# Kernel tuning notes

Hardware: AMD Instinct MI355X
Metric: run time of the kernel (lower is better)

Reference implementation:

```python
import jax, jax.numpy as jnp
import numpy as np

B, N = 32, 512
NFEAT, NHID, NCLASS, NHEADS = 128, 64, 128, 8
WORK_D, SUB_D = 32, 32
H1, H2, OUT_D = 256, 256, 512
ALPHA = 0.2
NEG = -9e15


def setup_inputs() -> dict:
    key = jax.random.key(0)
    ks = jax.random.split(key, 16)
    return {
        "graph_inf": jax.random.normal(ks[0], (B, N, NFEAT), jnp.float32),
        "graph_matrix": jax.random.randint(ks[1], (B, N, N), 0, 2, jnp.int32),
        "masks": jnp.ones((B, N), jnp.float32),
        "node_order": jax.random.randint(ks[2], (B,), 0, N, jnp.int64),
        "work": jax.random.normal(ks[3], (B, WORK_D), jnp.float32),
        "subtask": jax.random.normal(ks[4], (B, SUB_D), jnp.float32),
        # GAT head params
        "W_heads": jax.random.normal(ks[5], (NHEADS, NFEAT, NHID), jnp.float32) * 0.1,
        "a_heads": jax.random.normal(ks[6], (NHEADS, 2 * NHID), jnp.float32) * 0.1,
        "W_out": jax.random.normal(ks[7], (NHID * NHEADS, NCLASS), jnp.float32) * 0.05,
        "a_out": jax.random.normal(ks[8], (2 * NCLASS,), jnp.float32) * 0.1,
        # MLP encoder params
        "fc1_w": jax.random.normal(ks[9], (NCLASS + WORK_D + SUB_D, H1), jnp.float32) * 0.07,
        "fc1_b": jnp.zeros((H1,), jnp.float32),
        "fc2_w": jax.random.normal(ks[10], (H1, H2), jnp.float32) * 0.06,
        "fc2_b": jnp.zeros((H2,), jnp.float32),
        "fc3_w": jax.random.normal(ks[11], (H2, OUT_D), jnp.float32) * 0.06,
        "fc3_b": jnp.zeros((OUT_D,), jnp.float32),
    }


def _gat_layer(Wh, a1, a2, adj, masks):
    # Wh: [B,N,F]; additive GAT score e_ij = leakyrelu(a1.Wh_i + a2.Wh_j)
    s1 = Wh @ a1  # [B,N]
    s2 = Wh @ a2  # [B,N]
    e = jax.nn.leaky_relu(s1[:, :, None] + s2[:, None, :], ALPHA)  # [B,N,N]
    att = jax.nn.softmax(jnp.where(adj > 0, e, NEG), axis=2)
    h_prime = jnp.einsum('bnm,bmf->bnf', att, Wh)
    return h_prime * masks[:, :, None]


def reference(graph_inf, graph_matrix, masks, node_order, work, subtask,
              W_heads, a_heads, W_out, a_out,
              fc1_w, fc1_b, fc2_w, fc2_b, fc3_w, fc3_b):
    adj = graph_matrix
    # multi-head GAT layer (concat=True -> ELU)
    def head(Wk, ak):
        Wh = jnp.einsum('bnf,fo->bno', graph_inf, Wk)
        return jax.nn.elu(_gat_layer(Wh, ak[:NHID], ak[NHID:], adj, masks))
    xh = jax.vmap(head)(W_heads, a_heads)  # [H,B,N,NHID]
    x = jnp.transpose(xh, (1, 2, 0, 3)).reshape(B, N, NHEADS * NHID)
    # output GAT layer (concat=False)
    Wh = jnp.einsum('bnf,fo->bno', x, W_out)
    x = _gat_layer(Wh, a_out[:NCLASS], a_out[NCLASS:], adj, masks)
    x = x * masks[:, :, None]
    # select subtask node per batch element
    selected = x[jnp.arange(B), node_order]  # [B,NCLASS]
    inf = jnp.concatenate([selected, work, subtask], axis=1)
    h = jax.nn.relu(inf @ fc1_w + fc1_b)
    h = jax.nn.relu(h @ fc2_w + fc2_b)
    out = h @ fc3_w + fc3_b
    return jax.nn.softmax(out, axis=-1)
```

## Files before the change

kernel.cpp:

```cpp
#include <hip/hip_runtime.h>

typedef unsigned short u16;
typedef unsigned int u32;
typedef unsigned long long u64;

typedef __bf16 bf16x8 __attribute__((ext_vector_type(8)));
typedef float f32x4 __attribute__((ext_vector_type(4)));

#define LOG2E 1.44269504088896340736f

__device__ __forceinline__ float b2f(u16 u) {
    u32 x = ((u32)u) << 16;
    return __builtin_bit_cast(float, x);
}
__device__ __forceinline__ u16 f2b(float f) {
    u32 u = __builtin_bit_cast(u32, f);
    u32 r = (u + 0x7fffu + ((u >> 16) & 1u)) >> 16;
    return (u16)r;
}
__device__ __forceinline__ float ld(const void* p, int i, bool bf) {
    return bf ? b2f(((const u16*)p)[i]) : ((const float*)p)[i];
}
__device__ __forceinline__ bool detect_bf16(const void* masks) {
    return ((const u16*)masks)[0] != 0;
}
__device__ __forceinline__ f32x4 mfma16(bf16x8 a, bf16x8 b, f32x4 c) {
    return __builtin_amdgcn_mfma_f32_16x16x32_bf16(a, b, c, 0, 0, 0);
}

__device__ __attribute__((aligned(256))) u32  g_adjm[16384 * 16];
__device__ __attribute__((aligned(256))) u16  g_BT1[512 * 128];
__device__ __attribute__((aligned(256))) u16  g_BT2[128 * 512];
__device__ __attribute__((aligned(256))) u16  g_Xc[32 * 512 * 128];
__device__ __attribute__((aligned(256))) u16  g_xb[16384 * 512];
__device__ __attribute__((aligned(256))) u16  g_Wh2[16384 * 128];
__device__ __attribute__((aligned(256))) float g_s1b[16384];
__device__ __attribute__((aligned(256))) float g_s2b[16384];
__device__ __attribute__((aligned(256))) u16  g_fc1T[256 * 192];
__device__ __attribute__((aligned(256))) u16  g_fc2T[256 * 256];
__device__ __attribute__((aligned(256))) u16  g_fc3T[512 * 256];
__device__ __attribute__((aligned(256))) u16  g_Ahi[32 * 192];
__device__ __attribute__((aligned(256))) u16  g_Alo[32 * 192];
__device__ __attribute__((aligned(256))) u16  g_H1hi[32 * 256];
__device__ __attribute__((aligned(256))) u16  g_H1lo[32 * 256];
__device__ __attribute__((aligned(256))) u16  g_H2hi[32 * 256];
__device__ __attribute__((aligned(256))) u16  g_H2lo[32 * 256];
__device__ __attribute__((aligned(256))) float g_logits[32 * 512];

__global__ __launch_bounds__(256) void prep_kernel(
    const int* __restrict__ adj, const void* __restrict__ Whd,
    const void* __restrict__ Wo, const void* __restrict__ Xin,
    const void* __restrict__ fc1w, const void* __restrict__ fc2w,
    const void* __restrict__ fc3w, const void* __restrict__ masks)
{
    const bool bf = detect_bf16(masks);
    const int blk = blockIdx.x;
    const int tid = threadIdx.x;
    if (blk < 1024) {
        int id = blk * 256 + tid;
        int row = id >> 4, w = id & 15;
        const int4* p = (const int4*)(adj + row * 512 + w * 32);
        int4 v[8];
        #pragma unroll
        for (int s = 0; s < 8; ++s) v[s] = p[s];
        u32 word = 0;
        #pragma unroll
        for (int s = 0; s < 8; ++s) {
            u32 nib = (v[s].x > 0 ? 1u : 0u) | (v[s].y > 0 ? 2u : 0u) |
                      (v[s].z > 0 ? 4u : 0u) | (v[s].w > 0 ? 8u : 0u);
            word |= nib << (4 * s);
        }
        g_adjm[id] = word;
    } else if (blk < 1028) {
        int base = (blk - 1024) * 16384;
        for (int e = base + tid; e < base + 16384; e += 256) {
            int n = e >> 7, k = e & 127;
            g_BT1[e] = f2b(ld(Whd, (n >> 6) * 8192 + k * 64 + (n & 63), bf));
        }
    } else if (blk < 1032) {
        int base = (blk - 1028) * 16384;
        for (int e = base + tid; e < base + 16384; e += 256) {
            int n = e >> 9, k = e & 511;
            g_BT2[e] = f2b(ld(Wo, k * 128 + n, bf));
        }
    } else if (blk < 1288) {
        if (!bf) {
            int base = (blk - 1032) * 8192;
            for (int e = base + tid; e < base + 8192; e += 256)
                g_Xc[e] = f2b(((const float*)Xin)[e]);
        }
    } else if (blk < 1294) {
        int base = (blk - 1288) * 8192;
        for (int e = base + tid; e < base + 8192; e += 256) {
            int n = e / 192, k = e - n * 192;
            g_fc1T[e] = f2b(ld(fc1w, k * 256 + n, bf));
        }
    } else if (blk < 1302) {
        int base = (blk - 1294) * 8192;
        for (int e = base + tid; e < base + 8192; e += 256) {
            int n = e >> 8, k = e & 255;
            g_fc2T[e] = f2b(ld(fc2w, k * 256 + n, bf));
        }
    } else {
        int base = (blk - 1302) * 8192;
        for (int e = base + tid; e < base + 8192; e += 256) {
            int n = e >> 8, k = e & 255;
            g_fc3T[e] = f2b(ld(fc3w, k * 512 + n, bf));
        }
    }
}

__global__ __launch_bounds__(512, 1) void gat1_kernel(
    const void* __restrict__ Xin, const void* __restrict__ a_heads,
    const void* __restrict__ masks)
{
    __shared__ __attribute__((aligned(16))) u16 WhL[64 * 520];
    __shared__ __attribute__((aligned(16))) u16 As[64 * 136];
    __shared__ __attribute__((aligned(16))) u16 XcL[128 * 136];
    __shared__ float s1p[4][512];
    __shared__ float s2p[4][512];
    __shared__ float E2s[512];
    __shared__ float E2ps[512];

    const bool bf = detect_bf16(masks);
    const int tid = threadIdx.x;
    const int w = tid >> 6, lane = tid & 63;
    const int c = lane & 15, q = lane >> 4;
    const int h  = blockIdx.x & 7;
    const int b  = blockIdx.x >> 3;

    const u16* Bsrc = bf ? (const u16*)Xin : g_Xc;

    {
        int r = tid >> 3, seg = (tid & 7) * 16;
        const u16* src = g_BT1 + (h * 64 + r) * 128 + seg;
        *(uint4*)&As[r * 136 + seg] = *(const uint4*)src;
        *(uint4*)&As[r * 136 + seg + 8] = *(const uint4*)(src + 8);
    }

    const int wm = w & 3, wn = w >> 2;
    float a1v[4], a2v[4];
    #pragma unroll
    for (int i = 0; i < 4; ++i) {
        int o = wm * 16 + q * 4 + i;
        a1v[i] = ld(a_heads, h * 128 + o, bf);
        a2v[i] = ld(a_heads, h * 128 + 64 + o, bf);
    }

    for (int chunk = 0; chunk < 4; ++chunk) {
        __syncthreads();
        {
            int r = tid >> 2, seg = (tid & 3) * 32;
            const u16* src = Bsrc + (b * 512 + chunk * 128 + r) * 128 + seg;
            u16* dst = &XcL[r * 136 + seg];
            *(uint4*)dst = *(const uint4*)src;
            *(uint4*)(dst + 8) = *(const uint4*)(src + 8);
            *(uint4*)(dst + 16) = *(const uint4*)(src + 16);
            *(uint4*)(dst + 24) = *(const uint4*)(src + 24);
        }
        __syncthreads();
        f32x4 cacc[4] = {};
        #pragma unroll
        for (int kt = 0; kt < 4; ++kt) {
            bf16x8 af = *(const bf16x8*)&As[(wm * 16 + c) * 136 + kt * 32 + q * 8];
            #pragma unroll
            for (int nt = 0; nt < 4; ++nt) {
                bf16x8 bv = *(const bf16x8*)&XcL[(wn * 64 + nt * 16 + c) * 136 + kt * 32 + q * 8];
                cacc[nt] = mfma16(af, bv, cacc[nt]);
            }
        }
        #pragma unroll
        for (int nt = 0; nt < 4; ++nt) {
            const int ncol = chunk * 128 + wn * 64 + nt * 16 + c;
            float p1 = 0.f, p2 = 0.f;
            #pragma unroll
            for (int i = 0; i < 4; ++i) {
                float v = cacc[nt][i];
                WhL[(wm * 16 + q * 4 + i) * 520 + ncol] = f2b(v);
                p1 += v * a1v[i];
                p2 += v * a2v[i];
            }
            p1 += __shfl_xor(p1, 16); p1 += __shfl_xor(p1, 32);
            p2 += __shfl_xor(p2, 16); p2 += __shfl_xor(p2, 32);
            if (lane < 16) {
                int n = chunk * 128 + wn * 64 + nt * 16 + lane;
                s1p[wm][n] = p1;
                s2p[wm][n] = p2;
            }
        }
    }
    __syncthreads();
    {
        float s2v = (s2p[0][tid & 511] + s2p[1][tid & 511] +
                     s2p[2][tid & 511] + s2p[3][tid & 511]) * LOG2E;
        if (tid < 512) {
            E2s[tid]  = exp2f(s2v);
            E2ps[tid] = exp2f(0.2f * s2v);
        }
    }
    __syncthreads();

    const u32* adjb = g_adjm + b * 8192;
    const u32 bword = (c == 0) ? 0x3F803F80u : 0u;
    const uint4 bq = {bword, bword, bword, bword};
    const bf16x8 bone = __builtin_bit_cast(bf16x8, bq);

    float E1[4], E1p[4];
    #pragma unroll
    for (int g = 0; g < 4; ++g) {
        int r = w * 64 + g * 16 + c;
        float s1v = (s1p[0][r] + s1p[1][r] + s1p[2][r] + s1p[3][r]) * LOG2E;
        E1[g]  = exp2f(s1v);
        E1p[g] = exp2f(0.2f * s1v);
    }

    f32x4 acc[4][4] = {};
    f32x4 acc1[4] = {};
    const u16* lbase = &WhL[c * 520 + q * 8];

    for (int kc = 0; kc < 4; ++kc) {
        union { uint4 v; u32 a[4]; } wq[4];
        #pragma unroll
        for (int g = 0; g < 4; ++g)
            wq[g].v = *(const uint4*)(adjb + (w * 64 + g * 16 + c) * 16 + kc * 4);
        #pragma unroll
        for (int tl = 0; tl < 4; ++tl) {
            const int jb = kc * 128 + tl * 32 + q * 8;
            union { float4 v[2]; float f[8]; } e2r, e2pr;
            e2r.v[0]  = *(const float4*)&E2s[jb];
            e2r.v[1]  = *(const float4*)&E2s[jb + 4];
            e2pr.v[0] = *(const float4*)&E2ps[jb];
            e2pr.v[1] = *(const float4*)&E2ps[jb + 4];
            bf16x8 bfrag[4];
            #pragma unroll
            for (int nt = 0; nt < 4; ++nt)
                bfrag[nt] = *(const bf16x8*)(lbase + nt * 16 * 520 + kc * 128 + tl * 32);
            #pragma unroll
            for (int g = 0; g < 4; ++g) {
                u32 wbits = wq[g].a[tl] >> (q * 8);
                u32 pk[4];
                #pragma unroll
                for (int pi = 0; pi < 4; ++pi) {
                    float z0 = fmaxf(E1[g] * e2r.f[2 * pi],     E1p[g] * e2pr.f[2 * pi]);
                    float z1 = fmaxf(E1[g] * e2r.f[2 * pi + 1], E1p[g] * e2pr.f[2 * pi + 1]);
                    z0 = ((wbits >> (2 * pi)) & 1u) ? z0 : 0.f;
                    z1 = ((wbits >> (2 * pi + 1)) & 1u) ? z1 : 0.f;
                    pk[pi] = __builtin_amdgcn_perm(__builtin_bit_cast(u32, z1),
                                                   __builtin_bit_cast(u32, z0),
                                                   0x07060302u);
                }
                uint4 pkv = {pk[0], pk[1], pk[2], pk[3]};
                bf16x8 pv = __builtin_bit_cast(bf16x8, pkv);
                acc1[g] = mfma16(pv, bone, acc1[g]);
                #pragma unroll
                for (int nt = 0; nt < 4; ++nt)
                    acc[g][nt] = mfma16(pv, bfrag[nt], acc[g][nt]);
            }
        }
    }
    #pragma unroll
    for (int g = 0; g < 4; ++g) {
        const int R = w * 64 + g * 16;
        #pragma unroll
        for (int i = 0; i < 4; ++i) {
            float lr = __shfl(acc1[g][i], (lane & 48));
            float invr = (lr == 0.f) ? (1.f / 512.f) : (1.f / lr);
            const int row = R + q * 4 + i;
            float mk = ld(masks, b * 512 + row, bf);
            #pragma unroll
            for (int nt = 0; nt < 4; ++nt) {
                float v = acc[g][nt][i] * invr * mk;
                float o = v > 0.f ? v : (__expf(v) - 1.f);
                g_xb[(b * 512 + row) * 512 + h * 64 + nt * 16 + c] = f2b(o);
            }
        }
    }
}

__global__ __launch_bounds__(256, 2) void gemm2_kernel(
    const void* __restrict__ a_out, const void* __restrict__ masks)
{
    __shared__ __attribute__((aligned(16))) u16 Asl[64 * 72];
    __shared__ __attribute__((aligned(16))) u16 Bsl[128 * 72];
    const int tid = threadIdx.x;
    const int w = tid >> 6, lane = tid & 63;
    const int c = lane & 15, q = lane >> 4;
    const int tm = blockIdx.x * 64;
    const int rowA = tid >> 2, shA = (tid & 3) * 16;
    const int rowB = tid >> 1, shB = (tid & 1) * 32;
    f32x4 acc[8] = {};
    for (int kc = 0; kc < 512; kc += 64) {
        __syncthreads();
        const u16* Ag = g_xb + (tm + rowA) * 512 + kc + shA;
        *(uint4*)&Asl[rowA * 72 + shA] = *(const uint4*)Ag;
        *(uint4*)&Asl[rowA * 72 + shA + 8] = *(const uint4*)(Ag + 8);
        const u16* Bg = g_BT2 + rowB * 512 + kc + shB;
        #pragma unroll
        for (int s = 0; s < 4; ++s)
            *(uint4*)&Bsl[rowB * 72 + shB + 8 * s] = *(const uint4*)(Bg + 8 * s);
        __syncthreads();
        #pragma unroll
        for (int kt = 0; kt < 2; ++kt) {
            bf16x8 av = *(const bf16x8*)&Asl[(w * 16 + c) * 72 + kt * 32 + q * 8];
            #pragma unroll
            for (int ct = 0; ct < 8; ++ct) {
                bf16x8 bv = *(const bf16x8*)&Bsl[(ct * 16 + c) * 72 + kt * 32 + q * 8];
                acc[ct] = mfma16(av, bv, acc[ct]);
            }
        }
    }
    const bool bf = detect_bf16(masks);
    float a1v[8], a2v[8];
    #pragma unroll
    for (int ct = 0; ct < 8; ++ct) {
        a1v[ct] = ld(a_out, ct * 16 + c, bf);
        a2v[ct] = ld(a_out, 128 + ct * 16 + c, bf);
    }
    #pragma unroll
    for (int i = 0; i < 4; ++i) {
        float p1 = 0.f, p2 = 0.f;
        #pragma unroll
        for (int ct = 0; ct < 8; ++ct) {
            p1 += acc[ct][i] * a1v[ct];
            p2 += acc[ct][i] * a2v[ct];
        }
        #pragma unroll
        for (int off = 1; off < 16; off <<= 1) {
            p1 += __shfl_xor(p1, off);
            p2 += __shfl_xor(p2, off);
        }
        if (c == 0) {
            int m = tm + w * 16 + q * 4 + i;
            g_s1b[m] = p1 * LOG2E;
            g_s2b[m] = p2 * LOG2E;
        }
    }
    #pragma unroll
    for (int ct = 0; ct < 8; ++ct)
        #pragma unroll
        for (int i = 0; i < 4; ++i) {
            int m = tm + w * 16 + q * 4 + i;
            g_Wh2[m * 128 + ct * 16 + c] = f2b(acc[ct][i]);
        }
}

__global__ __launch_bounds__(256) void fin_att(
    const void* __restrict__ masks, const int* __restrict__ node_order,
    const void* __restrict__ workv, const void* __restrict__ subtaskv)
{
    __shared__ float att[512];
    __shared__ float parts[16][128];
    __shared__ float redl[4];

    const bool bf = detect_bf16(masks);
    const int b = blockIdx.x, t = threadIdx.x;
    const int lane = t & 63, wv = t >> 6;
    const int istar = node_order[b];

    const float s1v = g_s1b[b * 512 + istar];
    const u32* arow = g_adjm + (b * 512 + istar) * 16;
    float ssum = 0.f;
    #pragma unroll
    for (int rep = 0; rep < 2; ++rep) {
        int j = t + rep * 256;
        float e = s1v + g_s2b[b * 512 + j];
        e = fmaxf(e, 0.2f * e);
        float ex = ((arow[j >> 5] >> (j & 31)) & 1u) ? exp2f(e) : 0.f;
        att[j] = ex;
        ssum += ex;
    }
    for (int off = 1; off < 64; off <<= 1) ssum += __shfl_xor(ssum, off);
    if (lane == 0) redl[wv] = ssum;
    __syncthreads();
    float tot = redl[0] + redl[1] + redl[2] + redl[3];
    bool uni = (tot == 0.f);
    float inv = uni ? (1.f / 512.f) : (1.f / tot);

    const int og = t & 15, jg = t >> 4;
    float acc[8] = {};
    const u16* base = g_Wh2 + (b * 512 + jg * 32) * 128 + og * 8;
    #pragma unroll 8
    for (int j0 = 0; j0 < 32; ++j0) {
        float wgt = uni ? 1.f : att[jg * 32 + j0];
        union { u16 u[8]; uint4 v; } z;
        z.v = *(const uint4*)(base + j0 * 128);
        #pragma unroll
        for (int i = 0; i < 8; ++i) acc[i] += wgt * b2f(z.u[i]);
    }
    #pragma unroll
    for (int i = 0; i < 8; ++i) parts[jg][og * 8 + i] = acc[i];
    __syncthreads();
    float mk = ld(masks, b * 512 + istar, bf);
    if (t < 128) {
        float s = 0.f;
        #pragma unroll
        for (int jj = 0; jj < 16; ++jj) s += parts[jj][t];
        s *= inv * mk * mk;
        u16 hi = f2b(s);
        g_Ahi[b * 192 + t] = hi;
        g_Alo[b * 192 + t] = f2b(s - b2f(hi));
    } else if (t < 160) {
        g_Ahi[b * 192 + t] = bf ? ((const u16*)workv)[b * 32 + t - 128]
                                : f2b(((const float*)workv)[b * 32 + t - 128]);
        g_Alo[b * 192 + t] = 0;
    } else if (t < 192) {
        g_Ahi[b * 192 + t] = bf ? ((const u16*)subtaskv)[b * 32 + t - 160]
                                : f2b(((const float*)subtaskv)[b * 32 + t - 160]);
        g_Alo[b * 192 + t] = 0;
    }
}

template<int K, int NOUT, bool RELU>
__device__ __forceinline__ void mlp_body(
    const u16* __restrict__ Ahi, const u16* __restrict__ Alo,
    const u16* __restrict__ WT, const void* __restrict__ bias,
    u16* __restrict__ Ohi, u16* __restrict__ Olo, float* __restrict__ Of,
    const void* __restrict__ masks)
{
    const bool bf = detect_bf16(masks);
    const int t = threadIdx.x, w = t >> 6, lane = t & 63;
    const int c = lane & 15, q = lane >> 4;
    const int col = blockIdx.x * 64 + w * 16 + c;

    const u16* wp  = WT + col * K + q * 8;
    const u16* ahp = Ahi + c * K + q * 8;
    const u16* alp = Alo + c * K + q * 8;

    f32x4 acc0 = {}, acc1 = {};
    #pragma unroll
    for (int kt = 0; kt < K / 32; ++kt) {
        bf16x8 bw  = *(const bf16x8*)(wp + kt * 32);
        bf16x8 ah0 = *(const bf16x8*)(ahp + kt * 32);
        bf16x8 al0 = *(const bf16x8*)(alp + kt * 32);
        bf16x8 ah1 = *(const bf16x8*)(ahp + 16 * K + kt * 32);
        bf16x8 al1 = *(const bf16x8*)(alp + 16 * K + kt * 32);
        acc0 = mfma16(ah0, bw, acc0);
        acc0 = mfma16(al0, bw, acc0);
        acc1 = mfma16(ah1, bw, acc1);
        acc1 = mfma16(al1, bw, acc1);
    }
    float bs = ld(bias, col, bf);
    #pragma unroll
    for (int mt = 0; mt < 2; ++mt) {
        f32x4 a = mt ? acc1 : acc0;
        #pragma unroll
        for (int i = 0; i < 4; ++i) {
            int m = mt * 16 + q * 4 + i;
            float v = a[i] + bs;
            if (RELU) {
                v = fmaxf(v, 0.f);
                u16 hi = f2b(v);
                Ohi[m * NOUT + col] = hi;
                Olo[m * NOUT + col] = f2b(v - b2f(hi));
            } else {
                Of[m * NOUT + col] = v;
            }
        }
    }
}

__global__ __launch_bounds__(256) void mlp1_kernel(const void* bias, const void* masks) {
    mlp_body<192, 256, true>(g_Ahi, g_Alo, g_fc1T, bias, g_H1hi, g_H1lo, nullptr, masks);
}
__global__ __launch_bounds__(256) void mlp2_kernel(const void* bias, const void* masks) {
    mlp_body<256, 256, true>(g_H1hi, g_H1lo, g_fc2T, bias, g_H2hi, g_H2lo, nullptr, masks);
}
__global__ __launch_bounds__(256) void mlp3_kernel(const void* bias, const void* masks) {
    mlp_body<256, 512, false>(g_H2hi, g_H2lo, g_fc3T, bias, nullptr, nullptr, g_logits, masks);
}

__global__ __launch_bounds__(64) void softmax_kernel(
    const void* __restrict__ masks, void* __restrict__ out)
{
    const bool bf = detect_bf16(masks);
    const int row = blockIdx.x, lane = threadIdx.x;
    const float* lp = g_logits + row * 512 + lane * 8;
    float v[8];
    *(float4*)&v[0] = *(const float4*)lp;
    *(float4*)&v[4] = *(const float4*)(lp + 4);
    float mx = v[0];
    #pragma unroll
    for (int i = 1; i < 8; ++i) mx = fmaxf(mx, v[i]);
    for (int off = 1; off < 64; off <<= 1) mx = fmaxf(mx, __shfl_xor(mx, off));
    float e[8];
    float s = 0.f;
    #pragma unroll
    for (int i = 0; i < 8; ++i) { e[i] = __expf(v[i] - mx); s += e[i]; }
    for (int off = 1; off < 64; off <<= 1) s += __shfl_xor(s, off);
    float inv = 1.f / s;
    if (bf) {
        u16* o = (u16*)out + row * 512 + lane * 8;
        #pragma unroll
        for (int i = 0; i < 8; ++i) o[i] = f2b(e[i] * inv);
    } else {
        float* o = (float*)out + row * 512 + lane * 8;
        #pragma unroll
        for (int i = 0; i < 8; ++i) o[i] = e[i] * inv;
    }
}

extern "C" void kernel_launch(void* const* d_in, const int* in_sizes, int n_in,
                              void* d_out, int out_size, void* d_ws, size_t ws_size,
                              hipStream_t stream)
{
    const void* graph_inf    = d_in[0];
    const int*  graph_matrix = (const int*)d_in[1];
    const void* masks        = d_in[2];
    const int*  node_order   = (const int*)d_in[3];
    const void* work         = d_in[4];
    const void* subtask      = d_in[5];
    const void* W_heads      = d_in[6];
    const void* a_heads      = d_in[7];
    const void* W_out        = d_in[8];
    const void* a_out        = d_in[9];
    const void* fc1w         = d_in[10];
    const void* fc1b         = d_in[11];
    const void* fc2w         = d_in[12];
    const void* fc2b         = d_in[13];
    const void* fc3w         = d_in[14];
    const void* fc3b         = d_in[15];

    prep_kernel<<<dim3(1318), dim3(256), 0, stream>>>(graph_matrix, W_heads, W_out, graph_inf,
                                                      fc1w, fc2w, fc3w, masks);
    gat1_kernel<<<dim3(256), dim3(512), 0, stream>>>(graph_inf, a_heads, masks);
    gemm2_kernel<<<dim3(256), dim3(256), 0, stream>>>(a_out, masks);
    fin_att<<<dim3(32), dim3(256), 0, stream>>>(masks, node_order, work, subtask);
    mlp1_kernel<<<dim3(4), dim3(256), 0, stream>>>(fc1b, masks);
    mlp2_kernel<<<dim3(4), dim3(256), 0, stream>>>(fc2b, masks);
    mlp3_kernel<<<dim3(8), dim3(256), 0, stream>>>(fc3b, masks);
    softmax_kernel<<<dim3(32), dim3(64), 0, stream>>>(masks, d_out);
}
```

Baseline: 191.3 us.

## Double gat1 block to 1024 threads, prefetch X chunks in registers, remap block order

The GAT head kernel now runs 16 waves per block instead of 8, halving each wave's row groups in both the projection GEMM and the attention aggregation, which lowers register pressure and raises latency hiding. Loads of the next X chunk are issued into registers before the current chunk's MFMA work, so global latency overlaps compute. Block indexing puts batch in the low bits so consecutive blocks share a head's weights. The cost is more per-wave overhead from redundant B-fragment and E2 loads, and a higher chance of register spills under the 1024-thread bound.

```diff
diff --git a/kernel.cpp b/kernel.cpp
--- a/kernel.cpp
+++ b/kernel.cpp
@@ -110,7 +110,7 @@
     }
 }
 
-__global__ __launch_bounds__(512, 1) void gat1_kernel(
+__global__ __launch_bounds__(1024, 1) void gat1_kernel(
     const void* __restrict__ Xin, const void* __restrict__ a_heads,
     const void* __restrict__ masks)
 {
@@ -126,16 +126,14 @@
     const int tid = threadIdx.x;
     const int w = tid >> 6, lane = tid & 63;
     const int c = lane & 15, q = lane >> 4;
-    const int h  = blockIdx.x & 7;
-    const int b  = blockIdx.x >> 3;
+    const int b = blockIdx.x & 31;
+    const int h = blockIdx.x >> 5;
 
     const u16* Bsrc = bf ? (const u16*)Xin : g_Xc;
 
     {
-        int r = tid >> 3, seg = (tid & 7) * 16;
-        const u16* src = g_BT1 + (h * 64 + r) * 128 + seg;
-        *(uint4*)&As[r * 136 + seg] = *(const uint4*)src;
-        *(uint4*)&As[r * 136 + seg + 8] = *(const uint4*)(src + 8);
+        int r = tid >> 4, seg = (tid & 15) * 8;
+        *(uint4*)&As[r * 136 + seg] = *(const uint4*)(g_BT1 + (h * 64 + r) * 128 + seg);
     }
 
     const int wm = w & 3, wn = w >> 2;
@@ -147,31 +145,37 @@
         a2v[i] = ld(a_heads, h * 128 + 64 + o, bf);
     }
 
+    const int pr = tid >> 3, pseg = (tid & 7) * 16;
+    uint4 xr0, xr1;
+    {
+        const u16* src = Bsrc + (b * 512 + pr) * 128 + pseg;
+        xr0 = *(const uint4*)src;
+        xr1 = *(const uint4*)(src + 8);
+    }
+
     for (int chunk = 0; chunk < 4; ++chunk) {
         __syncthreads();
-        {
-            int r = tid >> 2, seg = (tid & 3) * 32;
-            const u16* src = Bsrc + (b * 512 + chunk * 128 + r) * 128 + seg;
-            u16* dst = &XcL[r * 136 + seg];
-            *(uint4*)dst = *(const uint4*)src;
-            *(uint4*)(dst + 8) = *(const uint4*)(src + 8);
-            *(uint4*)(dst + 16) = *(const uint4*)(src + 16);
-            *(uint4*)(dst + 24) = *(const uint4*)(src + 24);
+        *(uint4*)&XcL[pr * 136 + pseg] = xr0;
+        *(uint4*)&XcL[pr * 136 + pseg + 8] = xr1;
+        if (chunk < 3) {
+            const u16* src = Bsrc + (b * 512 + (chunk + 1) * 128 + pr) * 128 + pseg;
+            xr0 = *(const uint4*)src;
+            xr1 = *(const uint4*)(src + 8);
         }
         __syncthreads();
-        f32x4 cacc[4] = {};
+        f32x4 cacc[2] = {};
         #pragma unroll
         for (int kt = 0; kt < 4; ++kt) {
             bf16x8 af = *(const bf16x8*)&As[(wm * 16 + c) * 136 + kt * 32 + q * 8];
             #pragma unroll
-            for (int nt = 0; nt < 4; ++nt) {
-                bf16x8 bv = *(const bf16x8*)&XcL[(wn * 64 + nt * 16 + c) * 136 + kt * 32 + q * 8];
+            for (int nt = 0; nt < 2; ++nt) {
+                bf16x8 bv = *(const bf16x8*)&XcL[(wn * 32 + nt * 16 + c) * 136 + kt * 32 + q * 8];
                 cacc[nt] = mfma16(af, bv, cacc[nt]);
             }
         }
         #pragma unroll
-        for (int nt = 0; nt < 4; ++nt) {
-            const int ncol = chunk * 128 + wn * 64 + nt * 16 + c;
+        for (int nt = 0; nt < 2; ++nt) {
+            const int ncol = chunk * 128 + wn * 32 + nt * 16 + c;
             float p1 = 0.f, p2 = 0.f;
             #pragma unroll
             for (int i = 0; i < 4; ++i) {
@@ -183,7 +187,7 @@
             p1 += __shfl_xor(p1, 16); p1 += __shfl_xor(p1, 32);
             p2 += __shfl_xor(p2, 16); p2 += __shfl_xor(p2, 32);
             if (lane < 16) {
-                int n = chunk * 128 + wn * 64 + nt * 16 + lane;
+                int n = chunk * 128 + wn * 32 + nt * 16 + lane;
                 s1p[wm][n] = p1;
                 s2p[wm][n] = p2;
             }
@@ -191,12 +195,10 @@
     }
     __syncthreads();
     {
-        float s2v = (s2p[0][tid & 511] + s2p[1][tid & 511] +
-                     s2p[2][tid & 511] + s2p[3][tid & 511]) * LOG2E;
-        if (tid < 512) {
-            E2s[tid]  = exp2f(s2v);
-            E2ps[tid] = exp2f(0.2f * s2v);
-        }
+        int j = tid & 511;
+        float s2v = (s2p[0][j] + s2p[1][j] + s2p[2][j] + s2p[3][j]) * LOG2E;
+        if (tid < 512) E2s[j]  = exp2f(s2v);
+        else           E2ps[j] = exp2f(0.2f * s2v);
     }
     __syncthreads();
 
@@ -205,24 +207,24 @@
     const uint4 bq = {bword, bword, bword, bword};
     const bf16x8 bone = __builtin_bit_cast(bf16x8, bq);
 
-    float E1[4], E1p[4];
-    #pragma unroll
-    for (int g = 0; g < 4; ++g) {
-        int r = w * 64 + g * 16 + c;
+    float E1[2], E1p[2];
+    #pragma unroll
+    for (int g = 0; g < 2; ++g) {
+        int r = w * 32 + g * 16 + c;
         float s1v = (s1p[0][r] + s1p[1][r] + s1p[2][r] + s1p[3][r]) * LOG2E;
         E1[g]  = exp2f(s1v);
         E1p[g] = exp2f(0.2f * s1v);
     }
 
-    f32x4 acc[4][4] = {};
-    f32x4 acc1[4] = {};
+    f32x4 acc[2][4] = {};
+    f32x4 acc1[2] = {};
     const u16* lbase = &WhL[c * 520 + q * 8];
 
     for (int kc = 0; kc < 4; ++kc) {
-        union { uint4 v; u32 a[4]; } wq[4];
-        #pragma unroll
-        for (int g = 0; g < 4; ++g)
-            wq[g].v = *(const uint4*)(adjb + (w * 64 + g * 16 + c) * 16 + kc * 4);
+        union { uint4 v; u32 a[4]; } wq[2];
+        #pragma unroll
+        for (int g = 0; g < 2; ++g)
+            wq[g].v = *(const uint4*)(adjb + (w * 32 + g * 16 + c) * 16 + kc * 4);
         #pragma unroll
         for (int tl = 0; tl < 4; ++tl) {
             const int jb = kc * 128 + tl * 32 + q * 8;
@@ -236,7 +238,7 @@
             for (int nt = 0; nt < 4; ++nt)
                 bfrag[nt] = *(const bf16x8*)(lbase + nt * 16 * 520 + kc * 128 + tl * 32);
             #pragma unroll
-            for (int g = 0; g < 4; ++g) {
+            for (int g = 0; g < 2; ++g) {
                 u32 wbits = wq[g].a[tl] >> (q * 8);
                 u32 pk[4];
                 #pragma unroll
@@ -259,8 +261,8 @@
         }
     }
     #pragma unroll
-    for (int g = 0; g < 4; ++g) {
-        const int R = w * 64 + g * 16;
+    for (int g = 0; g < 2; ++g) {
+        const int R = w * 32 + g * 16;
         #pragma unroll
         for (int i = 0; i < 4; ++i) {
             float lr = __shfl(acc1[g][i], (lane & 48));
@@ -522,7 +524,7 @@
 
     prep_kernel<<<dim3(1318), dim3(256), 0, stream>>>(graph_matrix, W_heads, W_out, graph_inf,
                                                       fc1w, fc2w, fc3w, masks);
-    gat1_kernel<<<dim3(256), dim3(512), 0, stream>>>(graph_inf, a_heads, masks);
+    gat1_kernel<<<dim3(256), dim3(1024), 0, stream>>>(graph_inf, a_heads, masks);
     gemm2_kernel<<<dim3(256), dim3(256), 0, stream>>>(a_out, masks);
     fin_att<<<dim3(32), dim3(256), 0, stream>>>(masks, node_order, work, subtask);
     mlp1_kernel<<<dim3(4), dim3(256), 0, stream>>>(fc1b, masks);
```

After: 184.4 us, median of 2. 1.04x faster.
